# Kernel optimization log

Measured on AMD Instinct MI355X. Metric: run time of the kernel, lower is better.

Reference implementation:

```python
import jax, jax.numpy as jnp
import numpy as np


def setup_inputs() -> dict:
    key = jax.random.key(0)
    k1, k2, k3 = jax.random.split(key, 3)
    N, M, H = 32768, 4096, 768
    fact = jax.random.normal(k1, (N, H), dtype=jnp.float32)
    elements_p = jax.random.normal(k2, (M, H), dtype=jnp.float32)
    # kaiming_uniform with a=sqrt(5) on [H,H]: bound = sqrt(6/((1+5)*H)) = 1/sqrt(H)
    bound = 1.0 / np.sqrt(H)
    weights = jax.random.uniform(k3, (H, H), dtype=jnp.float32, minval=-bound, maxval=bound)
    return {"fact": fact, "elements_p": elements_p, "weights": weights}


def reference(fact, elements_p, weights):
    # fact: [N,H], elements_p: [M,H], weights: [H,H]
    fact_Q = jnp.max(fact, axis=0, keepdims=True)                 # [1,H]
    f2e = (fact_Q @ weights) @ elements_p.T                        # [1,M]
    f2e = jax.nn.softmax(f2e, axis=-1)
    elements_p_ = jnp.sum(elements_p * f2e.T, axis=0, keepdims=True)  # [1,H]
    e2f = (fact @ weights) @ elements_p_.T                         # [N,1]
    e2f = jax.nn.softmax(e2f, axis=0)
    fact_ = jnp.sum(fact * e2f, axis=0, keepdims=True)             # [1,H]
    return (fact_, elements_p_)
```

## Files before the change

kernel.cpp:

```cpp
#include <hip/hip_runtime.h>
#include <math.h>


#define H 768
#define H4 192
#define PSTRIDE 772
#define ACC_OFF 4

__global__ __launch_bounds__(192) void k_colmax(const float4* __restrict__ x4,
                                                float4* __restrict__ pmax4, int N) {
  const int t = threadIdx.x;
  const int rpb = (N + gridDim.x - 1) / gridDim.x;
  const int n0 = blockIdx.x * rpb;
  const int n1 = min(N, n0 + rpb);
  float4 m = make_float4(-INFINITY, -INFINITY, -INFINITY, -INFINITY);
#pragma unroll 8
  for (int n = n0; n < n1; ++n) {
    float4 x = x4[(size_t)n * H4 + t];
    m.x = fmaxf(m.x, x.x); m.y = fmaxf(m.y, x.y);
    m.z = fmaxf(m.z, x.z); m.w = fmaxf(m.w, x.w);
  }
  pmax4[(size_t)blockIdx.x * H4 + t] = m;
}

__global__ __launch_bounds__(1024) void k_colreduce(const float* __restrict__ pmax,
                                                    float* __restrict__ fQ,
                                                    float* __restrict__ q, int B) {
  const int lane = threadIdx.x & 63;
  const int wv = threadIdx.x >> 6;
  const int c = blockIdx.x * 64 + lane;
  float m = -INFINITY;
#pragma unroll 4
  for (int b = wv; b < B; b += 16) m = fmaxf(m, pmax[(size_t)b * H + c]);
  __shared__ float s[16][64];
  s[wv][lane] = m;
  __syncthreads();
  if (wv == 0) {
    float mm = m;
#pragma unroll
    for (int w2 = 1; w2 < 16; ++w2) mm = fmaxf(mm, s[w2][lane]);
    fQ[c] = mm;
    q[c] = 0.f;
  }
}

__global__ __launch_bounds__(192) void k_q(const float4* __restrict__ W4,
                                           const float* __restrict__ fQ,
                                           float* __restrict__ q) {
  const int t = threadIdx.x;
  const int k0 = blockIdx.x * 16;
  float4 acc = make_float4(0.f, 0.f, 0.f, 0.f);
#pragma unroll 4
  for (int k = k0; k < k0 + 16; ++k) {
    const float f = fQ[k];
    const float4 w = W4[(size_t)k * H4 + t];
    acc.x = fmaf(f, w.x, acc.x);
    acc.y = fmaf(f, w.y, acc.y);
    acc.z = fmaf(f, w.z, acc.z);
    acc.w = fmaf(f, w.w, acc.w);
  }
  atomicAdd(&q[4 * t + 0], acc.x);
  atomicAdd(&q[4 * t + 1], acc.y);
  atomicAdd(&q[4 * t + 2], acc.z);
  atomicAdd(&q[4 * t + 3], acc.w);
}

template <int NW>
__global__ __launch_bounds__(NW * 64) void k_pass(const float4* __restrict__ X4,
                                                  const float* __restrict__ wv_,
                                                  float* __restrict__ part, int R) {
  const int lane = threadIdx.x & 63;
  const int wv = threadIdx.x >> 6;
  const int gw = blockIdx.x * NW + wv;
  const int nw = gridDim.x * NW;
  float4 wr[3];
#pragma unroll
  for (int j = 0; j < 3; ++j) wr[j] = ((const float4*)wv_)[lane + 64 * j];
  const int rpw = (R + nw - 1) / nw;
  const int r0 = gw * rpw;
  const int r1 = min(R, r0 + rpw);
  float mrun = -INFINITY, l = 0.f;
  float4 acc[3];
#pragma unroll
  for (int j = 0; j < 3; ++j) acc[j] = make_float4(0.f, 0.f, 0.f, 0.f);
  for (int r = r0; r < r1; ++r) {
    const float4* row = X4 + (size_t)r * H4;
    float4 x[3];
    float s = 0.f;
#pragma unroll
    for (int j = 0; j < 3; ++j) {
      x[j] = row[lane + 64 * j];
      s = fmaf(x[j].x, wr[j].x, s);
      s = fmaf(x[j].y, wr[j].y, s);
      s = fmaf(x[j].z, wr[j].z, s);
      s = fmaf(x[j].w, wr[j].w, s);
    }
#pragma unroll
    for (int o = 32; o; o >>= 1) s += __shfl_xor(s, o, 64);
    const float mn = fmaxf(mrun, s);
    const float esc = __expf(mrun - mn);
    const float p = __expf(s - mn);
    l = fmaf(l, esc, p);
#pragma unroll
    for (int j = 0; j < 3; ++j) {
      acc[j].x = fmaf(acc[j].x, esc, p * x[j].x);
      acc[j].y = fmaf(acc[j].y, esc, p * x[j].y);
      acc[j].z = fmaf(acc[j].z, esc, p * x[j].z);
      acc[j].w = fmaf(acc[j].w, esc, p * x[j].w);
    }
    mrun = mn;
  }
  __shared__ float sm[NW], sl[NW];
  __shared__ float4 sacc[NW][H4];
  if (lane == 0) { sm[wv] = mrun; sl[wv] = l; }
#pragma unroll
  for (int j = 0; j < 3; ++j) sacc[wv][lane + 64 * j] = acc[j];
  __syncthreads();
  if (wv == 0) {
    float gm = -INFINITY;
#pragma unroll
    for (int w2 = 0; w2 < NW; ++w2) gm = fmaxf(gm, sm[w2]);
    float fa[NW];
    float L = 0.f;
#pragma unroll
    for (int w2 = 0; w2 < NW; ++w2) {
      fa[w2] = (sl[w2] > 0.f) ? __expf(sm[w2] - gm) : 0.f;
      L = fmaf(fa[w2], sl[w2], L);
    }
    float* pb = part + (size_t)blockIdx.x * PSTRIDE;
#pragma unroll
    for (int j = 0; j < 3; ++j) {
      float4 a = make_float4(0.f, 0.f, 0.f, 0.f);
#pragma unroll
      for (int w2 = 0; w2 < NW; ++w2) {
        const float4 t = sacc[w2][lane + 64 * j];
        a.x = fmaf(fa[w2], t.x, a.x);
        a.y = fmaf(fa[w2], t.y, a.y);
        a.z = fmaf(fa[w2], t.z, a.z);
        a.w = fmaf(fa[w2], t.w, a.w);
      }
      *(float4*)(pb + ACC_OFF + 4 * (lane + 64 * j)) = a;
    }
    if (lane == 0) { pb[0] = gm; pb[1] = L; }
  }
}

__global__ __launch_bounds__(1024) void k_combine(const float* __restrict__ part, int B,
                                                  float* __restrict__ out0,
                                                  float* __restrict__ out1) {
  const int lane = threadIdx.x & 63;
  const int wv = threadIdx.x >> 6;
  __shared__ float sred[16];
  __shared__ float sacc[16][64];
  float gm = -INFINITY;
  for (int b = threadIdx.x; b < B; b += 1024) gm = fmaxf(gm, part[(size_t)b * PSTRIDE]);
#pragma unroll
  for (int o = 32; o; o >>= 1) gm = fmaxf(gm, __shfl_xor(gm, o, 64));
  if (lane == 0) sred[wv] = gm;
  __syncthreads();
  gm = sred[0];
#pragma unroll
  for (int w2 = 1; w2 < 16; ++w2) gm = fmaxf(gm, sred[w2]);
  __syncthreads();
  float L = 0.f;
  for (int b = threadIdx.x; b < B; b += 1024) {
    const float m = part[(size_t)b * PSTRIDE];
    const float lb = part[(size_t)b * PSTRIDE + 1];
    L = fmaf((lb > 0.f) ? __expf(m - gm) : 0.f, lb, L);
  }
#pragma unroll
  for (int o = 32; o; o >>= 1) L += __shfl_xor(L, o, 64);
  if (lane == 0) sred[wv] = L;
  const int c = blockIdx.x * 64 + lane;
  float a = 0.f;
  for (int b = wv; b < B; b += 16) {
    const float m = part[(size_t)b * PSTRIDE];
    const float lb = part[(size_t)b * PSTRIDE + 1];
    const float e = (lb > 0.f) ? __expf(m - gm) : 0.f;
    a = fmaf(e, part[(size_t)b * PSTRIDE + ACC_OFF + c], a);
  }
  sacc[wv][lane] = a;
  __syncthreads();
  if (wv == 0) {
    float s = 0.f, Lt = 0.f;
#pragma unroll
    for (int w2 = 0; w2 < 16; ++w2) { s += sacc[w2][lane]; Lt += sred[w2]; }
    const float r = s / Lt;
    out0[c] = r;
    if (out1) out1[c] = r;
  }
}

__global__ __launch_bounds__(256) void k_v(const float4* __restrict__ W4,
                                           const float* __restrict__ ep_,
                                           float* __restrict__ v) {
  const int lane = threadIdx.x & 63;
  const int i = blockIdx.x * 4 + (threadIdx.x >> 6);
  float s = 0.f;
#pragma unroll
  for (int j = 0; j < 3; ++j) {
    const float4 w = W4[(size_t)i * H4 + lane + 64 * j];
    const float4 e = ((const float4*)ep_)[lane + 64 * j];
    s = fmaf(w.x, e.x, s);
    s = fmaf(w.y, e.y, s);
    s = fmaf(w.z, e.z, s);
    s = fmaf(w.w, e.w, s);
  }
#pragma unroll
  for (int o = 32; o; o >>= 1) s += __shfl_xor(s, o, 64);
  if (lane == 0) v[i] = s;
}

extern "C" void kernel_launch(void* const* d_in, const int* in_sizes, int n_in,
                              void* d_out, int out_size, void* d_ws, size_t ws_size,
                              hipStream_t stream) {
  const float* fact = (const float*)d_in[0];
  const float* ep   = (const float*)d_in[1];
  const float* W    = (const float*)d_in[2];
  float* out = (float*)d_out;
  const int N = in_sizes[0] / H;
  const int M = in_sizes[1] / H;

  const int B1 = 1024;
  const int BM = 256;
  const int BN = 1024;

  float* wsf  = (float*)d_ws;
  float* fQ   = wsf;
  float* q    = wsf + 768;
  float* v    = wsf + 1536;
  float* epws = wsf + 2304;
  float* pmax = wsf + 3072;
  float* pm   = pmax + (size_t)B1 * H;
  float* pn   = pm + (size_t)BM * PSTRIDE;

  k_colmax<<<B1, 192, 0, stream>>>((const float4*)fact, (float4*)pmax, N);
  k_colreduce<<<12, 1024, 0, stream>>>(pmax, fQ, q, B1);
  k_q<<<48, 192, 0, stream>>>((const float4*)W, fQ, q);
  k_pass<8><<<BM, 512, 0, stream>>>((const float4*)ep, q, pm, M);
  k_combine<<<12, 1024, 0, stream>>>(pm, BM, out + H, epws);
  k_v<<<192, 256, 0, stream>>>((const float4*)W, epws, v);
  k_pass<8><<<BN, 512, 0, stream>>>((const float4*)fact, v, pn, N);
  k_combine<<<12, 1024, 0, stream>>>(pn, BN, out, nullptr);
}
```

Measured before the change: 264.2 us.

## Fuse column reduce into k_q and combine into k_pass via last-block counter

Folds the column-max reduction into the q-projection kernel and the final softmax combine into the pass kernel, using an atomic counter so the last finishing block does the cross-block merge. The goal is fewer kernel launches and less launch and serialisation overhead. It also shrinks the grid sizes (colmax 1024→256, passes 256/1024→128/256), which cuts the partials that must be merged. In exchange it adds a memset for the counters and q, and leaves a serial tail where a single block does the combine.

```diff
diff --git a/kernel.cpp b/kernel.cpp
--- a/kernel.cpp
+++ b/kernel.cpp
@@ -23,171 +23,197 @@
   pmax4[(size_t)blockIdx.x * H4 + t] = m;
 }
 
-__global__ __launch_bounds__(1024) void k_colreduce(const float* __restrict__ pmax,
-                                                    float* __restrict__ fQ,
-                                                    float* __restrict__ q, int B) {
-  const int lane = threadIdx.x & 63;
-  const int wv = threadIdx.x >> 6;
-  const int c = blockIdx.x * 64 + lane;
-  float m = -INFINITY;
-#pragma unroll 4
-  for (int b = wv; b < B; b += 16) m = fmaxf(m, pmax[(size_t)b * H + c]);
-  __shared__ float s[16][64];
-  s[wv][lane] = m;
-  __syncthreads();
-  if (wv == 0) {
-    float mm = m;
-#pragma unroll
-    for (int w2 = 1; w2 < 16; ++w2) mm = fmaxf(mm, s[w2][lane]);
-    fQ[c] = mm;
-    q[c] = 0.f;
-  }
-}
-
 __global__ __launch_bounds__(192) void k_q(const float4* __restrict__ W4,
-                                           const float* __restrict__ fQ,
-                                           float* __restrict__ q) {
-  const int t = threadIdx.x;
+                                           const float* __restrict__ pmax,
+                                           float* __restrict__ q, int B) {
+  const int tid = threadIdx.x;
   const int k0 = blockIdx.x * 16;
+  __shared__ float sA[12][16];
+  __shared__ float fQl[16];
+  {
+    const int col = tid & 15;
+    const int grp = tid >> 4;
+    float m = -INFINITY;
+    for (int p = grp; p < B; p += 12) m = fmaxf(m, pmax[(size_t)p * H + k0 + col]);
+    sA[grp][col] = m;
+    __syncthreads();
+    if (tid < 16) {
+      float mm = sA[0][tid];
+#pragma unroll
+      for (int g = 1; g < 12; ++g) mm = fmaxf(mm, sA[g][tid]);
+      fQl[tid] = mm;
+    }
+    __syncthreads();
+  }
   float4 acc = make_float4(0.f, 0.f, 0.f, 0.f);
 #pragma unroll 4
-  for (int k = k0; k < k0 + 16; ++k) {
-    const float f = fQ[k];
-    const float4 w = W4[(size_t)k * H4 + t];
+  for (int kk = 0; kk < 16; ++kk) {
+    const float f = fQl[kk];
+    const float4 w = W4[(size_t)(k0 + kk) * H4 + tid];
     acc.x = fmaf(f, w.x, acc.x);
     acc.y = fmaf(f, w.y, acc.y);
     acc.z = fmaf(f, w.z, acc.z);
     acc.w = fmaf(f, w.w, acc.w);
   }
-  atomicAdd(&q[4 * t + 0], acc.x);
-  atomicAdd(&q[4 * t + 1], acc.y);
-  atomicAdd(&q[4 * t + 2], acc.z);
-  atomicAdd(&q[4 * t + 3], acc.w);
+  atomicAdd(&q[4 * tid + 0], acc.x);
+  atomicAdd(&q[4 * tid + 1], acc.y);
+  atomicAdd(&q[4 * tid + 2], acc.z);
+  atomicAdd(&q[4 * tid + 3], acc.w);
 }
 
 template <int NW>
 __global__ __launch_bounds__(NW * 64) void k_pass(const float4* __restrict__ X4,
-                                                  const float* __restrict__ wv_,
-                                                  float* __restrict__ part, int R) {
+                                                  const float* __restrict__ wvec,
+                                                  float* __restrict__ part, int R,
+                                                  unsigned int* __restrict__ cnt,
+                                                  float* __restrict__ outA,
+                                                  float* __restrict__ outB) {
   const int lane = threadIdx.x & 63;
   const int wv = threadIdx.x >> 6;
-  const int gw = blockIdx.x * NW + wv;
-  const int nw = gridDim.x * NW;
-  float4 wr[3];
-#pragma unroll
-  for (int j = 0; j < 3; ++j) wr[j] = ((const float4*)wv_)[lane + 64 * j];
-  const int rpw = (R + nw - 1) / nw;
-  const int r0 = gw * rpw;
-  const int r1 = min(R, r0 + rpw);
-  float mrun = -INFINITY, l = 0.f;
-  float4 acc[3];
-#pragma unroll
-  for (int j = 0; j < 3; ++j) acc[j] = make_float4(0.f, 0.f, 0.f, 0.f);
-  for (int r = r0; r < r1; ++r) {
-    const float4* row = X4 + (size_t)r * H4;
-    float4 x[3];
-    float s = 0.f;
-#pragma unroll
-    for (int j = 0; j < 3; ++j) {
-      x[j] = row[lane + 64 * j];
-      s = fmaf(x[j].x, wr[j].x, s);
-      s = fmaf(x[j].y, wr[j].y, s);
-      s = fmaf(x[j].z, wr[j].z, s);
-      s = fmaf(x[j].w, wr[j].w, s);
-    }
-#pragma unroll
-    for (int o = 32; o; o >>= 1) s += __shfl_xor(s, o, 64);
-    const float mn = fmaxf(mrun, s);
-    const float esc = __expf(mrun - mn);
-    const float p = __expf(s - mn);
-    l = fmaf(l, esc, p);
-#pragma unroll
-    for (int j = 0; j < 3; ++j) {
-      acc[j].x = fmaf(acc[j].x, esc, p * x[j].x);
-      acc[j].y = fmaf(acc[j].y, esc, p * x[j].y);
-      acc[j].z = fmaf(acc[j].z, esc, p * x[j].z);
-      acc[j].w = fmaf(acc[j].w, esc, p * x[j].w);
-    }
-    mrun = mn;
-  }
+  const int NB = gridDim.x;
   __shared__ float sm[NW], sl[NW];
   __shared__ float4 sacc[NW][H4];
-  if (lane == 0) { sm[wv] = mrun; sl[wv] = l; }
-#pragma unroll
-  for (int j = 0; j < 3; ++j) sacc[wv][lane + 64 * j] = acc[j];
+
+  {
+    const int gw = blockIdx.x * NW + wv;
+    const int nw = NB * NW;
+    float4 wr[3];
+#pragma unroll
+    for (int j = 0; j < 3; ++j) wr[j] = ((const float4*)wvec)[lane + 64 * j];
+    const int rpw = (R + nw - 1) / nw;
+    const int r0 = gw * rpw;
+    const int r1 = min(R, r0 + rpw);
+    float mrun = -INFINITY, l = 0.f;
+    float4 acc[3];
+#pragma unroll
+    for (int j = 0; j < 3; ++j) acc[j] = make_float4(0.f, 0.f, 0.f, 0.f);
+    for (int r = r0; r < r1; ++r) {
+      const float4* row = X4 + (size_t)r * H4;
+      float4 x[3];
+      float s = 0.f;
+#pragma unroll
+      for (int j = 0; j < 3; ++j) {
+        x[j] = row[lane + 64 * j];
+        s = fmaf(x[j].x, wr[j].x, s);
+        s = fmaf(x[j].y, wr[j].y, s);
+        s = fmaf(x[j].z, wr[j].z, s);
+        s = fmaf(x[j].w, wr[j].w, s);
+      }
+#pragma unroll
+      for (int o = 32; o; o >>= 1) s += __shfl_xor(s, o, 64);
+      const float mn = fmaxf(mrun, s);
+      const float esc = __expf(mrun - mn);
+      const float p = __expf(s - mn);
+      l = fmaf(l, esc, p);
+#pragma unroll
+      for (int j = 0; j < 3; ++j) {
+        acc[j].x = fmaf(acc[j].x, esc, p * x[j].x);
+        acc[j].y = fmaf(acc[j].y, esc, p * x[j].y);
+        acc[j].z = fmaf(acc[j].z, esc, p * x[j].z);
+        acc[j].w = fmaf(acc[j].w, esc, p * x[j].w);
+      }
+      mrun = mn;
+    }
+    if (lane == 0) { sm[wv] = mrun; sl[wv] = l; }
+#pragma unroll
+    for (int j = 0; j < 3; ++j) sacc[wv][lane + 64 * j] = acc[j];
+    __syncthreads();
+    if (wv == 0) {
+      float gm = -INFINITY;
+#pragma unroll
+      for (int w2 = 0; w2 < NW; ++w2) gm = fmaxf(gm, sm[w2]);
+      float fa[NW];
+      float L = 0.f;
+#pragma unroll
+      for (int w2 = 0; w2 < NW; ++w2) {
+        fa[w2] = (sl[w2] > 0.f) ? __expf(sm[w2] - gm) : 0.f;
+        L = fmaf(fa[w2], sl[w2], L);
+      }
+      float* pb = part + (size_t)blockIdx.x * PSTRIDE;
+#pragma unroll
+      for (int j = 0; j < 3; ++j) {
+        float4 a = make_float4(0.f, 0.f, 0.f, 0.f);
+#pragma unroll
+        for (int w2 = 0; w2 < NW; ++w2) {
+          const float4 t = sacc[w2][lane + 64 * j];
+          a.x = fmaf(fa[w2], t.x, a.x);
+          a.y = fmaf(fa[w2], t.y, a.y);
+          a.z = fmaf(fa[w2], t.z, a.z);
+          a.w = fmaf(fa[w2], t.w, a.w);
+        }
+        *(float4*)(pb + ACC_OFF + 4 * (lane + 64 * j)) = a;
+      }
+      if (lane == 0) { pb[0] = gm; pb[1] = L; }
+    }
+  }
+
   __syncthreads();
-  if (wv == 0) {
+  __shared__ unsigned int s_last;
+  if (threadIdx.x == 0) {
+    __threadfence();
+    s_last = atomicAdd(cnt, 1u);
+  }
+  __syncthreads();
+  if (s_last != (unsigned)(NB - 1)) return;
+  __threadfence();
+
+  {
+    __shared__ float sred[NW];
+    const float* P = part;
     float gm = -INFINITY;
-#pragma unroll
-    for (int w2 = 0; w2 < NW; ++w2) gm = fmaxf(gm, sm[w2]);
-    float fa[NW];
+    for (int b = threadIdx.x; b < NB; b += NW * 64) gm = fmaxf(gm, P[(size_t)b * PSTRIDE]);
+#pragma unroll
+    for (int o = 32; o; o >>= 1) gm = fmaxf(gm, __shfl_xor(gm, o, 64));
+    if (lane == 0) sred[wv] = gm;
+    __syncthreads();
+    gm = sred[0];
+#pragma unroll
+    for (int w2 = 1; w2 < NW; ++w2) gm = fmaxf(gm, sred[w2]);
+    __syncthreads();
     float L = 0.f;
-#pragma unroll
-    for (int w2 = 0; w2 < NW; ++w2) {
-      fa[w2] = (sl[w2] > 0.f) ? __expf(sm[w2] - gm) : 0.f;
-      L = fmaf(fa[w2], sl[w2], L);
-    }
-    float* pb = part + (size_t)blockIdx.x * PSTRIDE;
-#pragma unroll
-    for (int j = 0; j < 3; ++j) {
-      float4 a = make_float4(0.f, 0.f, 0.f, 0.f);
-#pragma unroll
-      for (int w2 = 0; w2 < NW; ++w2) {
-        const float4 t = sacc[w2][lane + 64 * j];
-        a.x = fmaf(fa[w2], t.x, a.x);
-        a.y = fmaf(fa[w2], t.y, a.y);
-        a.z = fmaf(fa[w2], t.z, a.z);
-        a.w = fmaf(fa[w2], t.w, a.w);
-      }
-      *(float4*)(pb + ACC_OFF + 4 * (lane + 64 * j)) = a;
-    }
-    if (lane == 0) { pb[0] = gm; pb[1] = L; }
-  }
-}
-
-__global__ __launch_bounds__(1024) void k_combine(const float* __restrict__ part, int B,
-                                                  float* __restrict__ out0,
-                                                  float* __restrict__ out1) {
-  const int lane = threadIdx.x & 63;
-  const int wv = threadIdx.x >> 6;
-  __shared__ float sred[16];
-  __shared__ float sacc[16][64];
-  float gm = -INFINITY;
-  for (int b = threadIdx.x; b < B; b += 1024) gm = fmaxf(gm, part[(size_t)b * PSTRIDE]);
-#pragma unroll
-  for (int o = 32; o; o >>= 1) gm = fmaxf(gm, __shfl_xor(gm, o, 64));
-  if (lane == 0) sred[wv] = gm;
-  __syncthreads();
-  gm = sred[0];
-#pragma unroll
-  for (int w2 = 1; w2 < 16; ++w2) gm = fmaxf(gm, sred[w2]);
-  __syncthreads();
-  float L = 0.f;
-  for (int b = threadIdx.x; b < B; b += 1024) {
-    const float m = part[(size_t)b * PSTRIDE];
-    const float lb = part[(size_t)b * PSTRIDE + 1];
-    L = fmaf((lb > 0.f) ? __expf(m - gm) : 0.f, lb, L);
-  }
-#pragma unroll
-  for (int o = 32; o; o >>= 1) L += __shfl_xor(L, o, 64);
-  if (lane == 0) sred[wv] = L;
-  const int c = blockIdx.x * 64 + lane;
-  float a = 0.f;
-  for (int b = wv; b < B; b += 16) {
-    const float m = part[(size_t)b * PSTRIDE];
-    const float lb = part[(size_t)b * PSTRIDE + 1];
-    const float e = (lb > 0.f) ? __expf(m - gm) : 0.f;
-    a = fmaf(e, part[(size_t)b * PSTRIDE + ACC_OFF + c], a);
-  }
-  sacc[wv][lane] = a;
-  __syncthreads();
-  if (wv == 0) {
-    float s = 0.f, Lt = 0.f;
-#pragma unroll
-    for (int w2 = 0; w2 < 16; ++w2) { s += sacc[w2][lane]; Lt += sred[w2]; }
-    const float r = s / Lt;
-    out0[c] = r;
-    if (out1) out1[c] = r;
+    for (int b = threadIdx.x; b < NB; b += NW * 64) {
+      const float m = P[(size_t)b * PSTRIDE];
+      const float lb = P[(size_t)b * PSTRIDE + 1];
+      L = fmaf((lb > 0.f) ? __expf(m - gm) : 0.f, lb, L);
+    }
+#pragma unroll
+    for (int o = 32; o; o >>= 1) L += __shfl_xor(L, o, 64);
+    if (lane == 0) sred[wv] = L;
+    float4 a[3];
+#pragma unroll
+    for (int j = 0; j < 3; ++j) a[j] = make_float4(0.f, 0.f, 0.f, 0.f);
+    for (int b = wv; b < NB; b += NW) {
+      const float m = P[(size_t)b * PSTRIDE];
+      const float lb = P[(size_t)b * PSTRIDE + 1];
+      const float e = (lb > 0.f) ? __expf(m - gm) : 0.f;
+      const float4* pa = (const float4*)(P + (size_t)b * PSTRIDE + ACC_OFF);
+#pragma unroll
+      for (int j = 0; j < 3; ++j) {
+        const float4 t = pa[lane + 64 * j];
+        a[j].x = fmaf(e, t.x, a[j].x);
+        a[j].y = fmaf(e, t.y, a[j].y);
+        a[j].z = fmaf(e, t.z, a[j].z);
+        a[j].w = fmaf(e, t.w, a[j].w);
+      }
+    }
+#pragma unroll
+    for (int j = 0; j < 3; ++j) sacc[wv][lane + 64 * j] = a[j];
+    __syncthreads();
+    if (threadIdx.x < H4) {
+      float4 s = sacc[0][threadIdx.x];
+#pragma unroll
+      for (int w2 = 1; w2 < NW; ++w2) {
+        const float4 t = sacc[w2][threadIdx.x];
+        s.x += t.x; s.y += t.y; s.z += t.z; s.w += t.w;
+      }
+      float Lt = sred[0];
+#pragma unroll
+      for (int w2 = 1; w2 < NW; ++w2) Lt += sred[w2];
+      const float inv = 1.f / Lt;
+      const float4 r = make_float4(s.x * inv, s.y * inv, s.z * inv, s.w * inv);
+      ((float4*)outA)[threadIdx.x] = r;
+      if (outB) ((float4*)outB)[threadIdx.x] = r;
+    }
   }
 }
 
@@ -221,25 +247,24 @@
   const int N = in_sizes[0] / H;
   const int M = in_sizes[1] / H;
 
-  const int B1 = 1024;
-  const int BM = 256;
-  const int BN = 1024;
+  const int B1 = 256;
+  const int BM = 128;
+  const int BN = 256;
 
   float* wsf  = (float*)d_ws;
-  float* fQ   = wsf;
-  float* q    = wsf + 768;
-  float* v    = wsf + 1536;
-  float* epws = wsf + 2304;
-  float* pmax = wsf + 3072;
+  unsigned int* cnt2 = (unsigned int*)d_ws;
+  unsigned int* cnt3 = (unsigned int*)d_ws + 1;
+  float* q    = wsf + 4;
+  float* epws = wsf + 772;
+  float* v    = wsf + 1540;
+  float* pmax = wsf + 2308;
   float* pm   = pmax + (size_t)B1 * H;
   float* pn   = pm + (size_t)BM * PSTRIDE;
 
+  hipMemsetAsync(d_ws, 0, 3088, stream);
   k_colmax<<<B1, 192, 0, stream>>>((const float4*)fact, (float4*)pmax, N);
-  k_colreduce<<<12, 1024, 0, stream>>>(pmax, fQ, q, B1);
-  k_q<<<48, 192, 0, stream>>>((const float4*)W, fQ, q);
-  k_pass<8><<<BM, 512, 0, stream>>>((const float4*)ep, q, pm, M);
-  k_combine<<<12, 1024, 0, stream>>>(pm, BM, out + H, epws);
+  k_q<<<48, 192, 0, stream>>>((const float4*)W, pmax, q, B1);
+  k_pass<8><<<BM, 512, 0, stream>>>((const float4*)ep, q, pm, M, cnt2, epws, out + H);
   k_v<<<192, 256, 0, stream>>>((const float4*)W, epws, v);
-  k_pass<8><<<BN, 512, 0, stream>>>((const float4*)fact, v, pn, N);
-  k_combine<<<12, 1024, 0, stream>>>(pn, BN, out, nullptr);
-}
+  k_pass<8><<<BN, 512, 0, stream>>>((const float4*)fact, v, pn, N, cnt3, out, nullptr);
+}
```

Result: faster. 241.0 us (-8.8%).
